# Kernel tuning notes

Measured on AMD Instinct MI355X. Metric: run time of the kernel, lower is better.

## Reference

```python
import jax, jax.numpy as jnp
import numpy as np

EMBED_DIM = 128
NUM_HEADS = 4
HEAD_DIM = EMBED_DIM // NUM_HEADS


def setup_inputs() -> dict:
    key = jax.random.key(0)
    ks = jax.random.split(key, 12)
    B, N, D = 4, 4096, EMBED_DIM
    s = 1.0 / np.sqrt(D)
    inp = {
        "query": jax.random.normal(ks[0], (B, N, D), dtype=jnp.float32),
        "key": jax.random.normal(ks[1], (B, N, D), dtype=jnp.float32),
        "value": jax.random.normal(ks[2], (B, N, D), dtype=jnp.float32),
        "Wq": jax.random.uniform(ks[3], (D, D), jnp.float32, -s, s),
        "bq": jax.random.uniform(ks[4], (D,), jnp.float32, -s, s),
        "Wk": jax.random.uniform(ks[5], (D, D), jnp.float32, -s, s),
        "bk": jax.random.uniform(ks[6], (D,), jnp.float32, -s, s),
        "Wv": jax.random.uniform(ks[7], (D, D), jnp.float32, -s, s),
        "bv": jax.random.uniform(ks[8], (D,), jnp.float32, -s, s),
        "Wo": jax.random.uniform(ks[9], (D, D), jnp.float32, -s, s),
        "bo": jax.random.uniform(ks[10], (D,), jnp.float32, -s, s),
    }
    return inp


def reference(query, key, value, Wq, bq, Wk, bk, Wv, bv, Wo, bo):
    B, N, D = query.shape
    H, Dh = NUM_HEADS, HEAD_DIM
    scale = Dh ** -0.5
    # Linear projections (torch Linear: x @ W.T + b), split heads -> [B, H, N, Dh]
    Q = (query @ Wq.T + bq).reshape(B, N, H, Dh).transpose(0, 2, 1, 3)
    K = (key @ Wk.T + bk).reshape(B, N, H, Dh).transpose(0, 2, 1, 3)
    V = (value @ Wv.T + bv).reshape(B, N, H, Dh).transpose(0, 2, 1, 3)
    # Attention scores [B, H, N, N]
    scores = jnp.einsum('bhqd,bhkd->bhqk', Q, K) * scale
    attn = jax.nn.softmax(scores, axis=-1)
    ctx = jnp.einsum('bhqk,bhkd->bhqd', attn, V)  # [B, H, N, Dh]
    ctx = ctx.transpose(0, 2, 1, 3).reshape(B, N, D)
    return ctx @ Wo.T + bo
```

## Files before the change

### kernel.cpp

```cpp
#include <hip/hip_runtime.h>
#include <hip/hip_bf16.h>

#define N_SEQ 4096
#define DIM   128
#define NH    4
#define DH    32
#define BATCH 4

#define QSCALE 0.25503495870989204f

typedef __bf16 bf16x8 __attribute__((ext_vector_type(8)));
typedef __bf16 bf16x2 __attribute__((ext_vector_type(2)));
typedef __bf16 bf16x4 __attribute__((ext_vector_type(4)));
typedef float  f32x4  __attribute__((ext_vector_type(4)));

#define MFMA(a, b, c) __builtin_amdgcn_mfma_f32_16x16x32_bf16((a), (b), (c), 0, 0, 0)

static __device__ __forceinline__ bf16x8 cvt8(const float* __restrict__ p) {
    const float4* f4 = reinterpret_cast<const float4*>(p);
    float4 a = f4[0], b = f4[1];
    bf16x8 r;
    r[0] = (__bf16)a.x; r[1] = (__bf16)a.y; r[2] = (__bf16)a.z; r[3] = (__bf16)a.w;
    r[4] = (__bf16)b.x; r[5] = (__bf16)b.y; r[6] = (__bf16)b.z; r[7] = (__bf16)b.w;
    return r;
}

__global__ __launch_bounds__(256) void proj_qkv(
    const float* __restrict__ xq, const float* __restrict__ xk, const float* __restrict__ xv,
    const float* __restrict__ Wq, const float* __restrict__ Wk, const float* __restrict__ Wv,
    const float* __restrict__ bq, const float* __restrict__ bk, const float* __restrict__ bv,
    __bf16* __restrict__ Qs, __bf16* __restrict__ Kb, __bf16* __restrict__ Vt)
{
    __shared__ __align__(16) char wlds[34816];
    const int z = blockIdx.z;
    const float* x    = (z == 0) ? xq : ((z == 1) ? xk : xv);
    const float* Wf   = (z == 0) ? Wq : ((z == 1) ? Wk : Wv);
    const float* bias = (z == 0) ? bq : ((z == 1) ? bk : bv);
    const int b    = blockIdx.y;
    const int tid  = threadIdx.x;
    const int wave = tid >> 6, lane = tid & 63;
    const int quad = lane >> 4, l15 = lane & 15;
    const int n0   = blockIdx.x * 64 + wave * 16;

    {
        const int r = tid >> 1, half = tid & 1;
        const float* wsrc = Wf + r * DIM + half * 64;
        char* wdst = wlds + r * 272 + half * 128;
        #pragma unroll
        for (int i = 0; i < 8; i++)
            *(bf16x8*)(wdst + i * 16) = cvt8(wsrc + i * 8);
    }

    bf16x8 a[4];
    const float* xrow = x + (b * N_SEQ + n0 + l15) * DIM + quad * 8;
    a[0] = cvt8(xrow);      a[1] = cvt8(xrow + 32);
    a[2] = cvt8(xrow + 64); a[3] = cvt8(xrow + 96);
    __syncthreads();

    const int n = n0 + l15;
    for (int t = 0; t < 8; t++) {
        const char* wr = wlds + (t * 16 + l15) * 272 + quad * 16;
        bf16x8 w0 = *(const bf16x8*)(wr);
        bf16x8 w1 = *(const bf16x8*)(wr + 64);
        bf16x8 w2 = *(const bf16x8*)(wr + 128);
        bf16x8 w3 = *(const bf16x8*)(wr + 192);

        f32x4 acc = {0.f, 0.f, 0.f, 0.f};
        acc = MFMA(w0, a[0], acc);
        acc = MFMA(w1, a[1], acc);
        acc = MFMA(w2, a[2], acc);
        acc = MFMA(w3, a[3], acc);

        const int d0 = t * 16 + quad * 4;
        if (z == 0) {
            const int h = d0 >> 5, dh0 = d0 & 31;
            bf16x4 q4;
            #pragma unroll
            for (int r = 0; r < 4; r++)
                q4[r] = (__bf16)((acc[r] + bias[d0 + r]) * QSCALE);
            *(bf16x4*)(Qs + ((b * NH + h) * N_SEQ + n) * DH + dh0) = q4;
        } else if (z == 1) {
            const int h = d0 >> 5, dh0 = d0 & 31;
            bf16x4 k4;
            #pragma unroll
            for (int r = 0; r < 4; r++)
                k4[r] = (__bf16)(acc[r] + bias[d0 + r]);
            *(bf16x4*)(Kb + ((b * NH + h) * N_SEQ + n) * DH + dh0) = k4;
        } else {
            const int nl = n & 63;
            const int np = (n & ~63) | (nl & 35) | ((nl & 12) << 1) | ((nl & 16) >> 2);
            #pragma unroll
            for (int r = 0; r < 4; r++) {
                const int d = d0 + r, h = d >> 5, dh = d & 31;
                Vt[((b * NH + h) * DH + dh) * N_SEQ + np] = (__bf16)(acc[r] + bias[d]);
            }
        }
    }
}

__global__ __launch_bounds__(256, 2) void flash_attn(
    const __bf16* __restrict__ Qs, const __bf16* __restrict__ Kb,
    const __bf16* __restrict__ Vt, __bf16* __restrict__ ctxb)
{
    __shared__ __align__(16) char smem[19456];
    char* const Kbase = smem;
    char* const Vbase = smem + 10240;

    const int bid  = blockIdx.x;
    const int bh   = bid & 15;
    const int qc   = bid >> 4;
    const int tid  = threadIdx.x;
    const int wave = tid >> 6, lane = tid & 63;
    const int quad = lane >> 4, l15 = lane & 15;
    const int n0   = qc * 128 + wave * 32;

    const __bf16* Qp = Qs + (bh * N_SEQ + n0) * DH;
    bf16x8 qf0 = *(const bf16x8*)(Qp + l15 * DH + quad * 8);
    bf16x8 qf1 = *(const bf16x8*)(Qp + (16 + l15) * DH + quad * 8);

    const __bf16* gK = Kb + (size_t)bh * N_SEQ * DH + tid * 8;
    const __bf16* gV = Vt + ((size_t)bh * DH + (tid >> 3)) * N_SEQ + (tid & 7) * 8;
    const int kofsK = (tid >> 2) * 80 + (tid & 3) * 16;
    const int kofsV = (tid >> 3) * 144 + (tid & 7) * 16;

    {
        bf16x8 kr = *(const bf16x8*)(gK);
        bf16x8 vr = *(const bf16x8*)(gV);
        *(bf16x8*)(Kbase + kofsK) = kr;
        *(bf16x8*)(Vbase + kofsV) = vr;
    }
    __syncthreads();

    f32x4 c00 = {0.f,0.f,0.f,0.f}, c01 = {0.f,0.f,0.f,0.f};
    f32x4 c10 = {0.f,0.f,0.f,0.f}, c11 = {0.f,0.f,0.f,0.f};
    float l0 = 0.f, l1 = 0.f;
    const f32x4 z4 = {0.f,0.f,0.f,0.f};

    for (int kb = 0; kb < N_SEQ / 64; kb++) {
        const int cur = kb & 1;
        const char* Kc = Kbase + cur * 5120;
        const char* Vc = Vbase + cur * 4608;

        const int kn = (kb + 1) & (N_SEQ / 64 - 1);
        bf16x8 krn = *(const bf16x8*)(gK + kn * 64 * DH);
        bf16x8 vrn = *(const bf16x8*)(gV + kn * 64);

        bf16x8 kf0 = *(const bf16x8*)(Kc + l15 * 80 + quad * 16);
        bf16x8 kf1 = *(const bf16x8*)(Kc + (16 + l15) * 80 + quad * 16);
        bf16x8 kf2 = *(const bf16x8*)(Kc + (32 + l15) * 80 + quad * 16);
        bf16x8 kf3 = *(const bf16x8*)(Kc + (48 + l15) * 80 + quad * 16);

        f32x4 s00 = MFMA(kf0, qf0, z4), s10 = MFMA(kf1, qf0, z4);
        f32x4 s20 = MFMA(kf2, qf0, z4), s30 = MFMA(kf3, qf0, z4);
        f32x4 s01 = MFMA(kf0, qf1, z4), s11 = MFMA(kf1, qf1, z4);
        f32x4 s21 = MFMA(kf2, qf1, z4), s31 = MFMA(kf3, qf1, z4);

        bf16x8 pf00, pf10, pf01, pf11;
        #pragma unroll
        for (int r = 0; r < 4; r++) {
            float p0 = __builtin_amdgcn_exp2f(s00[r]);
            float p1 = __builtin_amdgcn_exp2f(s10[r]);
            float p2 = __builtin_amdgcn_exp2f(s20[r]);
            float p3 = __builtin_amdgcn_exp2f(s30[r]);
            l0 += (p0 + p1) + (p2 + p3);
            pf00[r] = (__bf16)p0; pf00[4 + r] = (__bf16)p1;
            pf10[r] = (__bf16)p2; pf10[4 + r] = (__bf16)p3;
        }
        #pragma unroll
        for (int r = 0; r < 4; r++) {
            float p0 = __builtin_amdgcn_exp2f(s01[r]);
            float p1 = __builtin_amdgcn_exp2f(s11[r]);
            float p2 = __builtin_amdgcn_exp2f(s21[r]);
            float p3 = __builtin_amdgcn_exp2f(s31[r]);
            l1 += (p0 + p1) + (p2 + p3);
            pf01[r] = (__bf16)p0; pf01[4 + r] = (__bf16)p1;
            pf11[r] = (__bf16)p2; pf11[4 + r] = (__bf16)p3;
        }

        bf16x8 vf00 = *(const bf16x8*)(Vc + l15 * 144 + quad * 16);
        bf16x8 vf10 = *(const bf16x8*)(Vc + (16 + l15) * 144 + quad * 16);
        bf16x8 vf01 = *(const bf16x8*)(Vc + l15 * 144 + 64 + quad * 16);
        bf16x8 vf11 = *(const bf16x8*)(Vc + (16 + l15) * 144 + 64 + quad * 16);

        c00 = MFMA(vf00, pf00, c00); c01 = MFMA(vf10, pf00, c01);
        c00 = MFMA(vf01, pf10, c00); c01 = MFMA(vf11, pf10, c01);
        c10 = MFMA(vf00, pf01, c10); c11 = MFMA(vf10, pf01, c11);
        c10 = MFMA(vf01, pf11, c10); c11 = MFMA(vf11, pf11, c11);

        *(bf16x8*)(Kbase + (cur ^ 1) * 5120 + kofsK) = krn;
        *(bf16x8*)(Vbase + (cur ^ 1) * 4608 + kofsV) = vrn;
        __syncthreads();
    }

    l0 += __shfl_xor(l0, 16); l0 += __shfl_xor(l0, 32);
    l1 += __shfl_xor(l1, 16); l1 += __shfl_xor(l1, 32);
    const float inv0 = 1.0f / l0, inv1 = 1.0f / l1;

    const int b = bh >> 2, h = bh & 3;
    #pragma unroll
    for (int qt = 0; qt < 2; qt++) {
        const float inv = qt ? inv1 : inv0;
        const int q = n0 + qt * 16 + l15;
        #pragma unroll
        for (int dt = 0; dt < 2; dt++) {
            f32x4 cc = qt ? (dt ? c11 : c10) : (dt ? c01 : c00);
            __bf16* dst = ctxb + ((size_t)(b * N_SEQ + q)) * DIM + h * DH + dt * 16 + quad * 4;
            bf16x2 e0 = {(__bf16)(cc[0] * inv), (__bf16)(cc[1] * inv)};
            bf16x2 e1 = {(__bf16)(cc[2] * inv), (__bf16)(cc[3] * inv)};
            *(bf16x2*)(dst)     = e0;
            *(bf16x2*)(dst + 2) = e1;
        }
    }
}

__global__ __launch_bounds__(256) void out_proj(
    const __bf16* __restrict__ ctxb, const float* __restrict__ Wo,
    const float* __restrict__ bo, float* __restrict__ out)
{
    __shared__ __align__(16) char wlds[34816];
    const int b    = blockIdx.y;
    const int tid  = threadIdx.x;
    const int wave = tid >> 6, lane = tid & 63;
    const int quad = lane >> 4, l15 = lane & 15;
    const int n0   = blockIdx.x * 64 + wave * 16;

    {
        const int r = tid >> 1, half = tid & 1;
        const float* wsrc = Wo + r * DIM + half * 64;
        char* wdst = wlds + r * 272 + half * 128;
        #pragma unroll
        for (int i = 0; i < 8; i++)
            *(bf16x8*)(wdst + i * 16) = cvt8(wsrc + i * 8);
    }

    bf16x8 a[4];
    const __bf16* crow = ctxb + (b * N_SEQ + n0 + l15) * DIM + quad * 8;
    a[0] = *(const bf16x8*)(crow);
    a[1] = *(const bf16x8*)(crow + 32);
    a[2] = *(const bf16x8*)(crow + 64);
    a[3] = *(const bf16x8*)(crow + 96);
    __syncthreads();

    const int n = n0 + l15;
    for (int t = 0; t < 8; t++) {
        const char* wr = wlds + (t * 16 + l15) * 272 + quad * 16;
        bf16x8 w0 = *(const bf16x8*)(wr);
        bf16x8 w1 = *(const bf16x8*)(wr + 64);
        bf16x8 w2 = *(const bf16x8*)(wr + 128);
        bf16x8 w3 = *(const bf16x8*)(wr + 192);

        f32x4 acc = {0.f, 0.f, 0.f, 0.f};
        acc = MFMA(w0, a[0], acc);
        acc = MFMA(w1, a[1], acc);
        acc = MFMA(w2, a[2], acc);
        acc = MFMA(w3, a[3], acc);

        const int d0 = t * 16 + quad * 4;
        float4 o;
        o.x = acc[0] + bo[d0];
        o.y = acc[1] + bo[d0 + 1];
        o.z = acc[2] + bo[d0 + 2];
        o.w = acc[3] + bo[d0 + 3];
        *(float4*)(out + (b * N_SEQ + n) * DIM + d0) = o;
    }
}

extern "C" void kernel_launch(void* const* d_in, const int* in_sizes, int n_in,
                              void* d_out, int out_size, void* d_ws, size_t ws_size,
                              hipStream_t stream)
{
    const float* query = (const float*)d_in[0];
    const float* key   = (const float*)d_in[1];
    const float* value = (const float*)d_in[2];
    const float* Wq = (const float*)d_in[3];
    const float* bq = (const float*)d_in[4];
    const float* Wk = (const float*)d_in[5];
    const float* bk = (const float*)d_in[6];
    const float* Wv = (const float*)d_in[7];
    const float* bv = (const float*)d_in[8];
    const float* Wo = (const float*)d_in[9];
    const float* bo = (const float*)d_in[10];
    float* out = (float*)d_out;

    char* ws = (char*)d_ws;
    const size_t e = (size_t)BATCH * N_SEQ * DIM;
    __bf16* Qs   = (__bf16*)(ws);
    __bf16* Kb   = (__bf16*)(ws + 2 * e);
    __bf16* Vt   = (__bf16*)(ws + 4 * e);
    __bf16* ctxb = (__bf16*)(ws + 6 * e);

    proj_qkv<<<dim3(64, BATCH, 3), 256, 0, stream>>>(
        query, key, value, Wq, Wk, Wv, bq, bk, bv, Qs, Kb, Vt);
    flash_attn<<<dim3(512), 256, 0, stream>>>(Qs, Kb, Vt, ctxb);
    out_proj<<<dim3(64, BATCH), 256, 0, stream>>>(ctxb, Wo, bo, out);
}
```

Measured before the change: 151.9 us.

## Compute softmax row sums with MFMA against ones and relayout V tile in LDS

Replaces the per-lane scalar accumulation of exponentials, and the final cross-lane shuffle reduction, with MFMA calls that multiply a vector of ones by the bf16 probability fragments. This moves the row-sum work from VALU onto the matrix unit. It also changes how V is staged into LDS so K and V share the same 80-byte row layout and store offsets, and the V buffer grows slightly. The cost is four extra MFMAs per tile, and the row sums are now taken from bf16-rounded probabilities, which slightly changes numerics.

New measurement: 160.2 us. +5.5%, slower.

```diff
diff --git a/kernel.cpp b/kernel.cpp
--- a/kernel.cpp
+++ b/kernel.cpp
@@ -23,6 +23,24 @@
     r[0] = (__bf16)a.x; r[1] = (__bf16)a.y; r[2] = (__bf16)a.z; r[3] = (__bf16)a.w;
     r[4] = (__bf16)b.x; r[5] = (__bf16)b.y; r[6] = (__bf16)b.z; r[7] = (__bf16)b.w;
     return r;
+}
+
+static __device__ __forceinline__ f32x4 exp4(f32x4 s) {
+    f32x4 r;
+    r[0] = __builtin_amdgcn_exp2f(s[0]);
+    r[1] = __builtin_amdgcn_exp2f(s[1]);
+    r[2] = __builtin_amdgcn_exp2f(s[2]);
+    r[3] = __builtin_amdgcn_exp2f(s[3]);
+    return r;
+}
+
+static __device__ __forceinline__ bf16x8 pack8(f32x4 a, f32x4 b) {
+    bf16x8 o;
+    o[0] = (__bf16)a[0]; o[1] = (__bf16)a[1];
+    o[2] = (__bf16)a[2]; o[3] = (__bf16)a[3];
+    o[4] = (__bf16)b[0]; o[5] = (__bf16)b[1];
+    o[6] = (__bf16)b[2]; o[7] = (__bf16)b[3];
+    return o;
 }
 
 __global__ __launch_bounds__(256) void proj_qkv(
@@ -102,7 +120,7 @@
     const __bf16* __restrict__ Qs, const __bf16* __restrict__ Kb,
     const __bf16* __restrict__ Vt, __bf16* __restrict__ ctxb)
 {
-    __shared__ __align__(16) char smem[19456];
+    __shared__ __align__(16) char smem[20480];
     char* const Kbase = smem;
     char* const Vbase = smem + 10240;
 
@@ -118,28 +136,33 @@
     bf16x8 qf0 = *(const bf16x8*)(Qp + l15 * DH + quad * 8);
     bf16x8 qf1 = *(const bf16x8*)(Qp + (16 + l15) * DH + quad * 8);
 
-    const __bf16* gK = Kb + (size_t)bh * N_SEQ * DH + tid * 8;
-    const __bf16* gV = Vt + ((size_t)bh * DH + (tid >> 3)) * N_SEQ + (tid & 7) * 8;
-    const int kofsK = (tid >> 2) * 80 + (tid & 3) * 16;
-    const int kofsV = (tid >> 3) * 144 + (tid & 7) * 16;
+    const int r_ = tid >> 2, c_ = tid & 3;
+    const __bf16* gK = Kb + (size_t)bh * N_SEQ * DH + r_ * DH + c_ * 8;
+    const int vd = ((r_ >> 4) & 1) * 16 + (r_ & 15);
+    const int vg = r_ >> 5;
+    const __bf16* gV = Vt + ((size_t)bh * DH + vd) * N_SEQ + vg * 32 + c_ * 8;
+    const int kofs = r_ * 80 + c_ * 16;
 
     {
         bf16x8 kr = *(const bf16x8*)(gK);
         bf16x8 vr = *(const bf16x8*)(gV);
-        *(bf16x8*)(Kbase + kofsK) = kr;
-        *(bf16x8*)(Vbase + kofsV) = vr;
+        *(bf16x8*)(Kbase + kofs) = kr;
+        *(bf16x8*)(Vbase + kofs) = vr;
     }
     __syncthreads();
 
     f32x4 c00 = {0.f,0.f,0.f,0.f}, c01 = {0.f,0.f,0.f,0.f};
     f32x4 c10 = {0.f,0.f,0.f,0.f}, c11 = {0.f,0.f,0.f,0.f};
-    float l0 = 0.f, l1 = 0.f;
+    f32x4 lac0 = {0.f,0.f,0.f,0.f}, lac1 = {0.f,0.f,0.f,0.f};
     const f32x4 z4 = {0.f,0.f,0.f,0.f};
+    bf16x8 ones;
+    #pragma unroll
+    for (int i = 0; i < 8; i++) ones[i] = (__bf16)1.0f;
 
     for (int kb = 0; kb < N_SEQ / 64; kb++) {
         const int cur = kb & 1;
         const char* Kc = Kbase + cur * 5120;
-        const char* Vc = Vbase + cur * 4608;
+        const char* Vc = Vbase + cur * 5120;
 
         const int kn = (kb + 1) & (N_SEQ / 64 - 1);
         bf16x8 krn = *(const bf16x8*)(gK + kn * 64 * DH);
@@ -155,46 +178,31 @@
         f32x4 s01 = MFMA(kf0, qf1, z4), s11 = MFMA(kf1, qf1, z4);
         f32x4 s21 = MFMA(kf2, qf1, z4), s31 = MFMA(kf3, qf1, z4);
 
-        bf16x8 pf00, pf10, pf01, pf11;
-        #pragma unroll
-        for (int r = 0; r < 4; r++) {
-            float p0 = __builtin_amdgcn_exp2f(s00[r]);
-            float p1 = __builtin_amdgcn_exp2f(s10[r]);
-            float p2 = __builtin_amdgcn_exp2f(s20[r]);
-            float p3 = __builtin_amdgcn_exp2f(s30[r]);
-            l0 += (p0 + p1) + (p2 + p3);
-            pf00[r] = (__bf16)p0; pf00[4 + r] = (__bf16)p1;
-            pf10[r] = (__bf16)p2; pf10[4 + r] = (__bf16)p3;
-        }
-        #pragma unroll
-        for (int r = 0; r < 4; r++) {
-            float p0 = __builtin_amdgcn_exp2f(s01[r]);
-            float p1 = __builtin_amdgcn_exp2f(s11[r]);
-            float p2 = __builtin_amdgcn_exp2f(s21[r]);
-            float p3 = __builtin_amdgcn_exp2f(s31[r]);
-            l1 += (p0 + p1) + (p2 + p3);
-            pf01[r] = (__bf16)p0; pf01[4 + r] = (__bf16)p1;
-            pf11[r] = (__bf16)p2; pf11[4 + r] = (__bf16)p3;
-        }
-
-        bf16x8 vf00 = *(const bf16x8*)(Vc + l15 * 144 + quad * 16);
-        bf16x8 vf10 = *(const bf16x8*)(Vc + (16 + l15) * 144 + quad * 16);
-        bf16x8 vf01 = *(const bf16x8*)(Vc + l15 * 144 + 64 + quad * 16);
-        bf16x8 vf11 = *(const bf16x8*)(Vc + (16 + l15) * 144 + 64 + quad * 16);
+        bf16x8 pf00 = pack8(exp4(s00), exp4(s10));
+        bf16x8 pf10 = pack8(exp4(s20), exp4(s30));
+        bf16x8 pf01 = pack8(exp4(s01), exp4(s11));
+        bf16x8 pf11 = pack8(exp4(s21), exp4(s31));
+
+        lac0 = MFMA(ones, pf00, lac0); lac0 = MFMA(ones, pf10, lac0);
+        lac1 = MFMA(ones, pf01, lac1); lac1 = MFMA(ones, pf11, lac1);
+
+        bf16x8 vf00 = *(const bf16x8*)(Vc + l15 * 80 + quad * 16);
+        bf16x8 vf10 = *(const bf16x8*)(Vc + (16 + l15) * 80 + quad * 16);
+        bf16x8 vf01 = *(const bf16x8*)(Vc + (32 + l15) * 80 + quad * 16);
+        bf16x8 vf11 = *(const bf16x8*)(Vc + (48 + l15) * 80 + quad * 16);
 
         c00 = MFMA(vf00, pf00, c00); c01 = MFMA(vf10, pf00, c01);
         c00 = MFMA(vf01, pf10, c00); c01 = MFMA(vf11, pf10, c01);
         c10 = MFMA(vf00, pf01, c10); c11 = MFMA(vf10, pf01, c11);
         c10 = MFMA(vf01, pf11, c10); c11 = MFMA(vf11, pf11, c11);
 
-        *(bf16x8*)(Kbase + (cur ^ 1) * 5120 + kofsK) = krn;
-        *(bf16x8*)(Vbase + (cur ^ 1) * 4608 + kofsV) = vrn;
+        *(bf16x8*)(Kbase + (cur ^ 1) * 5120 + kofs) = krn;
+        *(bf16x8*)(Vbase + (cur ^ 1) * 5120 + kofs) = vrn;
         __syncthreads();
     }
 
-    l0 += __shfl_xor(l0, 16); l0 += __shfl_xor(l0, 32);
-    l1 += __shfl_xor(l1, 16); l1 += __shfl_xor(l1, 32);
-    const float inv0 = 1.0f / l0, inv1 = 1.0f / l1;
+    const float inv0 = 1.0f / lac0[0];
+    const float inv1 = 1.0f / lac1[0];
 
     const int b = bh >> 2, h = bh & 3;
     #pragma unroll
```
